# Kernel optimization log

Measured on AMD Instinct MI355X. Metric: run time of the kernel, lower is better.

The kernel has to match this reference:

```python
import jax, jax.numpy as jnp
import numpy as np

L, B, H = 4096, 32, 512


def setup_inputs() -> dict:
    key = jax.random.key(0)
    k1, k2, k3, k4 = jax.random.split(key, 4)
    query = jax.random.normal(k1, (B, H), dtype=jnp.float32)
    key_val = jax.random.normal(k2, (L, B, H), dtype=jnp.float32)
    # torch Linear(2H, H, bias=False): weight is (H, 2H); we store transposed (2H, H)
    W = jax.random.normal(k3, (2 * H, H), dtype=jnp.float32) * (1.0 / np.sqrt(2 * H))
    v = jax.random.normal(k4, (H,), dtype=jnp.float32)
    return {"query": query, "key_val": key_val, "W": W, "v": v}


def reference(query, key_val, W, v):
    # concat([expand(query), key], -1) @ W == query @ W_q + key @ W_k
    Wq, Wk = W[:H], W[H:]                       # each (H, H)
    q_proj = query @ Wq                          # (B, H)
    k_proj = jnp.einsum('lbi,ih->lbh', key_val, Wk)  # (L, B, H)
    energy = jnp.tanh(q_proj[None, :, :] + k_proj)   # (L, B, H)
    scores = jnp.einsum('h,lbh->bl', v, energy)      # (B, L)
    return jax.nn.softmax(scores, axis=1)[:, None, :]  # (B, 1, L)
```

## Files before the change

kernel.cpp:

```cpp
#include <hip/hip_runtime.h>
#include <hip/hip_bf16.h>
#include <stdint.h>

#define L_DIM 4096
#define B_DIM 32
#define H_DIM 512
#define M_DIM (L_DIM * B_DIM)
#define K_DIM H_DIM

typedef _Float16 half8 __attribute__((ext_vector_type(8)));
typedef __fp16 fp16x2 __attribute__((ext_vector_type(2)));
typedef float floatx4 __attribute__((ext_vector_type(4)));

__device__ __forceinline__ float tanh_fast(float x) {
  float e = __builtin_amdgcn_exp2f(x * 2.88539008177793f);
  return 1.0f - 2.0f * __builtin_amdgcn_rcpf(e + 1.0f);
}

__device__ __forceinline__ uint2 pack4(const float4& f) {
  const fp16x2 p0 = __builtin_amdgcn_cvt_pkrtz(f.x, f.y);
  const fp16x2 p1 = __builtin_amdgcn_cvt_pkrtz(f.z, f.w);
  uint2 u;
  u.x = __builtin_bit_cast(unsigned, p0);
  u.y = __builtin_bit_cast(unsigned, p1);
  return u;
}

__global__ __launch_bounds__(512) void prep_kernel(const float* __restrict__ query,
                                                   const float* __restrict__ W,
                                                   float* __restrict__ qp,
                                                   _Float16* __restrict__ W2) {
  __shared__ float4 qred[512];
  if (blockIdx.x < 64) {
    const int t = blockIdx.x * 512 + threadIdx.x;
    const int l15 = t & 15;
    const int q = (t >> 4) & 3;
    const int nc = (t >> 6) & 31;
    const int kt = t >> 11;
    const int n = nc * 16 + l15;
    const int kbase = H_DIM + kt * 32 + q * 8;
    half8 h;
#pragma unroll
    for (int j = 0; j < 8; ++j)
      h[j] = (_Float16)W[(size_t)(kbase + j) * H_DIM + n];
    *(half8*)(W2 + (size_t)t * 8) = h;
  } else {
    const int b = blockIdx.x - 64;
    const int tid = threadIdx.x;
    const int hx = tid & 127;
    const int ky = tid >> 7;
    const int h = hx * 4;
    const float* qrow = query + b * H_DIM + ky * 128;
    const float* wrow = W + (size_t)(ky * 128) * H_DIM + h;
    float4 acc = make_float4(0.f, 0.f, 0.f, 0.f);
#pragma unroll 8
    for (int i = 0; i < 128; ++i) {
      const float qv = qrow[i];
      const float4 w4 = *(const float4*)(wrow + (size_t)i * H_DIM);
      acc.x += qv * w4.x; acc.y += qv * w4.y;
      acc.z += qv * w4.z; acc.w += qv * w4.w;
    }
    qred[tid] = acc;
    __syncthreads();
    if (ky == 0) {
      const float4 a1 = qred[tid + 128], a2 = qred[tid + 256], a3 = qred[tid + 384];
      acc.x += a1.x + a2.x + a3.x;
      acc.y += a1.y + a2.y + a3.y;
      acc.z += a1.z + a2.z + a3.z;
      acc.w += a1.w + a2.w + a3.w;
      *(float4*)(qp + (size_t)b * H_DIM + h) = acc;
    }
  }
}

__global__ __launch_bounds__(512, 4) void fused_gemm_kernel(
    const float* __restrict__ key, const _Float16* __restrict__ W2,
    const float* __restrict__ qp, const float* __restrict__ v,
    float* __restrict__ scores) {
  __shared__ __align__(16) _Float16 As[2][64 * 32];
  __shared__ float swave[8 * 64];

  const int tid = threadIdx.x;
  const int lane = tid & 63;
  const int wn = tid >> 6;
  const int l15 = lane & 15;
  const int quad = lane >> 4;
  const int m0 = blockIdx.x * 64;

  const int srow = tid >> 3;
  const int schunk = tid & 7;
  const float* ag = key + (size_t)(m0 + srow) * K_DIM + schunk * 4;
  const int adst = srow * 32 + schunk * 4;

  const half8* bptr = (const half8*)W2 + (size_t)(wn * 4) * 64 + lane;

  floatx4 acc[4][4];
#pragma unroll
  for (int fm = 0; fm < 4; ++fm)
#pragma unroll
    for (int fn = 0; fn < 4; ++fn) acc[fm][fn] = (floatx4)0.0f;

  half8 bn[2][4];

  float4 ra0 = *(const float4*)(ag);
  float4 rb[2];
  rb[1] = *(const float4*)(ag + 32);
  rb[0] = *(const float4*)(ag + 64);
#pragma unroll
  for (int fn = 0; fn < 4; ++fn) bn[0][fn] = bptr[fn * 64];
  bptr += 32 * 64;
  *(uint2*)(As[0] + adst) = pack4(ra0);
  asm volatile("s_waitcnt lgkmcnt(0)" ::: "memory");
  __builtin_amdgcn_s_barrier();
  __builtin_amdgcn_sched_barrier(0);

#pragma unroll
  for (int kt = 0; kt < 16; ++kt) {
    if (kt < 15) {
#pragma unroll
      for (int fn = 0; fn < 4; ++fn) bn[(kt + 1) & 1][fn] = bptr[fn * 64];
      bptr += 32 * 64;
    }

    const _Float16* buf = As[kt & 1];
    half8 av0 = *(const half8*)(buf + (0 * 16 + l15) * 32 + quad * 8);
    half8 av1 = *(const half8*)(buf + (1 * 16 + l15) * 32 + quad * 8);

    if (kt < 15) {
      *(uint2*)(As[(kt + 1) & 1] + adst) = pack4(rb[(kt + 1) & 1]);
      if (kt < 13) rb[(kt + 1) & 1] = *(const float4*)(ag + (kt + 3) * 32);
    }

#pragma unroll
    for (int fn = 0; fn < 4; ++fn)
      acc[0][fn] = __builtin_amdgcn_mfma_f32_16x16x32_f16(av0, bn[kt & 1][fn],
                                                          acc[0][fn], 0, 0, 0);
#pragma unroll
    for (int fn = 0; fn < 4; ++fn)
      acc[1][fn] = __builtin_amdgcn_mfma_f32_16x16x32_f16(av1, bn[kt & 1][fn],
                                                          acc[1][fn], 0, 0, 0);

    half8 av2 = *(const half8*)(buf + (2 * 16 + l15) * 32 + quad * 8);
    half8 av3 = *(const half8*)(buf + (3 * 16 + l15) * 32 + quad * 8);

#pragma unroll
    for (int fn = 0; fn < 4; ++fn)
      acc[2][fn] = __builtin_amdgcn_mfma_f32_16x16x32_f16(av2, bn[kt & 1][fn],
                                                          acc[2][fn], 0, 0, 0);
#pragma unroll
    for (int fn = 0; fn < 4; ++fn)
      acc[3][fn] = __builtin_amdgcn_mfma_f32_16x16x32_f16(av3, bn[kt & 1][fn],
                                                          acc[3][fn], 0, 0, 0);

    __builtin_amdgcn_sched_barrier(0);
    asm volatile("s_waitcnt lgkmcnt(0)" ::: "memory");
    __builtin_amdgcn_s_barrier();
    __builtin_amdgcn_sched_barrier(0);
  }

  float vv[4];
#pragma unroll
  for (int fn = 0; fn < 4; ++fn) vv[fn] = v[wn * 64 + fn * 16 + l15];

#pragma unroll
  for (int fm = 0; fm < 4; ++fm) {
#pragma unroll
    for (int r = 0; r < 4; ++r) {
      const int mrow = fm * 16 + quad * 4 + r;
      const float* qrow = qp + (size_t)(mrow & 31) * H_DIM;
      float rs = 0.f;
#pragma unroll
      for (int fn = 0; fn < 4; ++fn) {
        const int n = wn * 64 + fn * 16 + l15;
        const float x = qrow[n] + acc[fm][fn][r];
        rs += vv[fn] * tanh_fast(x);
      }
      rs += __shfl_xor(rs, 1);
      rs += __shfl_xor(rs, 2);
      rs += __shfl_xor(rs, 4);
      rs += __shfl_xor(rs, 8);
      if (l15 == 0) swave[wn * 64 + mrow] = rs;
    }
  }
  __syncthreads();
  if (tid < 64) {
    float s = 0.f;
#pragma unroll
    for (int j = 0; j < 8; ++j) s += swave[j * 64 + tid];
    const int m = m0 + tid;
    scores[(size_t)(m & 31) * L_DIM + (m >> 5)] = s;
  }
}

__global__ __launch_bounds__(256) void softmax_kernel(const float* __restrict__ scores,
                                                      float* __restrict__ out) {
  const int b = blockIdx.x;
  const int t = threadIdx.x;
  const int lane = t & 63;
  const int w = t >> 6;
  __shared__ float redm[4], reds[4];
  const float* srow = scores + (size_t)b * L_DIM;
  float s[16];
#pragma unroll
  for (int i = 0; i < 16; ++i) s[i] = srow[t + i * 256];
  float mx = s[0];
#pragma unroll
  for (int i = 1; i < 16; ++i) mx = fmaxf(mx, s[i]);
#pragma unroll
  for (int off = 1; off < 64; off <<= 1) mx = fmaxf(mx, __shfl_xor(mx, off));
  if (lane == 0) redm[w] = mx;
  __syncthreads();
  mx = fmaxf(fmaxf(redm[0], redm[1]), fmaxf(redm[2], redm[3]));
  float sum = 0.f;
#pragma unroll
  for (int i = 0; i < 16; ++i) {
    s[i] = __builtin_amdgcn_exp2f((s[i] - mx) * 1.44269504f);
    sum += s[i];
  }
#pragma unroll
  for (int off = 1; off < 64; off <<= 1) sum += __shfl_xor(sum, off);
  if (lane == 0) reds[w] = sum;
  __syncthreads();
  const float inv = 1.0f / (reds[0] + reds[1] + reds[2] + reds[3]);
#pragma unroll
  for (int i = 0; i < 16; ++i) out[(size_t)b * L_DIM + t + i * 256] = s[i] * inv;
}

extern "C" void kernel_launch(void* const* d_in, const int* in_sizes, int n_in,
                              void* d_out, int out_size, void* d_ws, size_t ws_size,
                              hipStream_t stream) {
  const float* query = (const float*)d_in[0];
  const float* key   = (const float*)d_in[1];
  const float* W     = (const float*)d_in[2];
  const float* v     = (const float*)d_in[3];
  float* out = (float*)d_out;

  char* ws = (char*)d_ws;
  float* qp       = (float*)ws;
  float* scores   = (float*)(ws + 65536);
  _Float16* W2    = (_Float16*)(ws + 65536 + 524288);

  prep_kernel<<<96, 512, 0, stream>>>(query, W, qp, W2);
  fused_gemm_kernel<<<M_DIM / 64, 512, 0, stream>>>(key, W2, qp, v, scores);
  softmax_kernel<<<B_DIM, 256, 0, stream>>>(scores, out);
}
```

Measured before the change: 424.5 us.

## Stage 128-wide K slices in LDS with XOR swizzle to cut barriers

Each LDS stage now holds 128 K-columns (four MFMA k-steps) instead of 32, so the block synchronizes 3 times instead of 16 across the K loop. The global-to-LDS staging of key rows is spread over the four k-steps of each epoch with two rotating prefetch registers. An XOR swizzle on 16-byte column chunks is meant to avoid LDS bank conflicts on the wider rows. LDS per block grows from 8 KB to 32 KB, which may limit how many blocks fit per CU under the 4-blocks launch bound.

```diff
diff --git a/kernel.cpp b/kernel.cpp
--- a/kernel.cpp
+++ b/kernel.cpp
@@ -77,7 +77,7 @@
     const float* __restrict__ key, const _Float16* __restrict__ W2,
     const float* __restrict__ qp, const float* __restrict__ v,
     float* __restrict__ scores) {
-  __shared__ __align__(16) _Float16 As[2][64 * 32];
+  __shared__ __align__(16) _Float16 As[2][64 * 128];
   __shared__ float swave[8 * 64];
 
   const int tid = threadIdx.x;
@@ -88,9 +88,20 @@
   const int m0 = blockIdx.x * 64;
 
   const int srow = tid >> 3;
-  const int schunk = tid & 7;
-  const float* ag = key + (size_t)(m0 + srow) * K_DIM + schunk * 4;
-  const int adst = srow * 32 + schunk * 4;
+  const int ssub = tid & 7;
+  const float* ag = key + (size_t)(m0 + srow) * K_DIM + ssub * 4;
+
+  int wboff[4];
+#pragma unroll
+  for (int j = 0; j < 4; ++j)
+    wboff[j] = srow * 256 + (((j * 4 + (ssub >> 1)) ^ (srow & 7)) * 16) + (ssub & 1) * 8;
+
+  int rowoff[4];
+#pragma unroll
+  for (int fm = 0; fm < 4; ++fm) rowoff[fm] = (fm * 16 + l15) * 256;
+  int coff[4];
+#pragma unroll
+  for (int k4 = 0; k4 < 4; ++k4) coff[k4] = ((k4 * 4 + quad) ^ (l15 & 7)) * 16;
 
   const half8* bptr = (const half8*)W2 + (size_t)(wn * 4) * 64 + lane;
 
@@ -101,61 +112,81 @@
     for (int fn = 0; fn < 4; ++fn) acc[fm][fn] = (floatx4)0.0f;
 
   half8 bn[2][4];
-
-  float4 ra0 = *(const float4*)(ag);
-  float4 rb[2];
-  rb[1] = *(const float4*)(ag + 32);
-  rb[0] = *(const float4*)(ag + 64);
+  char* const lds = (char*)&As[0][0];
+
+  {
+    const float4 s0 = *(const float4*)(ag);
+    const float4 s1 = *(const float4*)(ag + 32);
+    const float4 s2 = *(const float4*)(ag + 64);
+    const float4 s3 = *(const float4*)(ag + 96);
+    *(uint2*)(lds + wboff[0]) = pack4(s0);
+    *(uint2*)(lds + wboff[1]) = pack4(s1);
+    *(uint2*)(lds + wboff[2]) = pack4(s2);
+    *(uint2*)(lds + wboff[3]) = pack4(s3);
+  }
+  float4 rbA = *(const float4*)(ag + 128);
+  float4 rbB = *(const float4*)(ag + 160);
 #pragma unroll
   for (int fn = 0; fn < 4; ++fn) bn[0][fn] = bptr[fn * 64];
   bptr += 32 * 64;
-  *(uint2*)(As[0] + adst) = pack4(ra0);
   asm volatile("s_waitcnt lgkmcnt(0)" ::: "memory");
   __builtin_amdgcn_s_barrier();
   __builtin_amdgcn_sched_barrier(0);
 
 #pragma unroll
-  for (int kt = 0; kt < 16; ++kt) {
-    if (kt < 15) {
-#pragma unroll
-      for (int fn = 0; fn < 4; ++fn) bn[(kt + 1) & 1][fn] = bptr[fn * 64];
-      bptr += 32 * 64;
-    }
-
-    const _Float16* buf = As[kt & 1];
-    half8 av0 = *(const half8*)(buf + (0 * 16 + l15) * 32 + quad * 8);
-    half8 av1 = *(const half8*)(buf + (1 * 16 + l15) * 32 + quad * 8);
-
-    if (kt < 15) {
-      *(uint2*)(As[(kt + 1) & 1] + adst) = pack4(rb[(kt + 1) & 1]);
-      if (kt < 13) rb[(kt + 1) & 1] = *(const float4*)(ag + (kt + 3) * 32);
-    }
-
-#pragma unroll
-    for (int fn = 0; fn < 4; ++fn)
-      acc[0][fn] = __builtin_amdgcn_mfma_f32_16x16x32_f16(av0, bn[kt & 1][fn],
-                                                          acc[0][fn], 0, 0, 0);
-#pragma unroll
-    for (int fn = 0; fn < 4; ++fn)
-      acc[1][fn] = __builtin_amdgcn_mfma_f32_16x16x32_f16(av1, bn[kt & 1][fn],
-                                                          acc[1][fn], 0, 0, 0);
-
-    half8 av2 = *(const half8*)(buf + (2 * 16 + l15) * 32 + quad * 8);
-    half8 av3 = *(const half8*)(buf + (3 * 16 + l15) * 32 + quad * 8);
-
-#pragma unroll
-    for (int fn = 0; fn < 4; ++fn)
-      acc[2][fn] = __builtin_amdgcn_mfma_f32_16x16x32_f16(av2, bn[kt & 1][fn],
-                                                          acc[2][fn], 0, 0, 0);
-#pragma unroll
-    for (int fn = 0; fn < 4; ++fn)
-      acc[3][fn] = __builtin_amdgcn_mfma_f32_16x16x32_f16(av3, bn[kt & 1][fn],
-                                                          acc[3][fn], 0, 0, 0);
-
-    __builtin_amdgcn_sched_barrier(0);
-    asm volatile("s_waitcnt lgkmcnt(0)" ::: "memory");
-    __builtin_amdgcn_s_barrier();
-    __builtin_amdgcn_sched_barrier(0);
+  for (int e = 0; e < 4; ++e) {
+    const char* rbase = lds + (e & 1) * 16384;
+    char* wbase = lds + ((e + 1) & 1) * 16384;
+#pragma unroll
+    for (int k4 = 0; k4 < 4; ++k4) {
+      const int kt = e * 4 + k4;
+      if (kt < 15) {
+#pragma unroll
+        for (int fn = 0; fn < 4; ++fn) bn[(kt + 1) & 1][fn] = bptr[fn * 64];
+        bptr += 32 * 64;
+      }
+
+      half8 av0 = *(const half8*)(rbase + rowoff[0] + coff[k4]);
+      half8 av1 = *(const half8*)(rbase + rowoff[1] + coff[k4]);
+
+      if (e < 3) {
+        if (k4 == 0) { *(uint2*)(wbase + wboff[0]) = pack4(rbA);
+                       rbA = *(const float4*)(ag + (e + 1) * 128 + 64); }
+        if (k4 == 1) { *(uint2*)(wbase + wboff[1]) = pack4(rbB);
+                       rbB = *(const float4*)(ag + (e + 1) * 128 + 96); }
+        if (k4 == 2) { *(uint2*)(wbase + wboff[2]) = pack4(rbA);
+                       if (e < 2) rbA = *(const float4*)(ag + (e + 2) * 128); }
+        if (k4 == 3) { *(uint2*)(wbase + wboff[3]) = pack4(rbB);
+                       if (e < 2) rbB = *(const float4*)(ag + (e + 2) * 128 + 32); }
+      }
+
+#pragma unroll
+      for (int fn = 0; fn < 4; ++fn)
+        acc[0][fn] = __builtin_amdgcn_mfma_f32_16x16x32_f16(av0, bn[kt & 1][fn],
+                                                            acc[0][fn], 0, 0, 0);
+#pragma unroll
+      for (int fn = 0; fn < 4; ++fn)
+        acc[1][fn] = __builtin_amdgcn_mfma_f32_16x16x32_f16(av1, bn[kt & 1][fn],
+                                                            acc[1][fn], 0, 0, 0);
+
+      half8 av2 = *(const half8*)(rbase + rowoff[2] + coff[k4]);
+      half8 av3 = *(const half8*)(rbase + rowoff[3] + coff[k4]);
+
+#pragma unroll
+      for (int fn = 0; fn < 4; ++fn)
+        acc[2][fn] = __builtin_amdgcn_mfma_f32_16x16x32_f16(av2, bn[kt & 1][fn],
+                                                            acc[2][fn], 0, 0, 0);
+#pragma unroll
+      for (int fn = 0; fn < 4; ++fn)
+        acc[3][fn] = __builtin_amdgcn_mfma_f32_16x16x32_f16(av3, bn[kt & 1][fn],
+                                                            acc[3][fn], 0, 0, 0);
+    }
+    if (e < 3) {
+      __builtin_amdgcn_sched_barrier(0);
+      asm volatile("s_waitcnt lgkmcnt(0)" ::: "memory");
+      __builtin_amdgcn_s_barrier();
+      __builtin_amdgcn_sched_barrier(0);
+    }
   }
 
   float vv[4];
```

After: 433.7 us. 1.02x slower.
